# Optimization experiments

Hardware: AMD Instinct MI355X
Metric: run time of the kernel (lower is better)

The kernel has to match this reference:

```python
import jax, jax.numpy as jnp
import numpy as np

EPS = 1e-5

def ln(x, g, b):
    m = x.mean(-1, keepdims=True)
    v = ((x - m) ** 2).mean(-1, keepdims=True)
    return (x - m) / jnp.sqrt(v + EPS) * g + b

def mha(x, in_w, in_b, out_w, out_b, nh):
    # Faithful nn.MultiheadAttention with batch_first=False: x is (L, B, D),
    # attention runs over axis 0 (sequence), axis 1 is batch.
    L, Bb, D = x.shape
    hd = D // nh
    qkv = x @ in_w.T + in_b                      # (L, B, 3D)
    q, k, v = jnp.split(qkv, 3, axis=-1)
    q = q.reshape(L, Bb, nh, hd) * (hd ** -0.5)
    k = k.reshape(L, Bb, nh, hd)
    v = v.reshape(L, Bb, nh, hd)
    a = jax.nn.softmax(jnp.einsum('lbhe,sbhe->bhls', q, k), axis=-1)
    o = jnp.einsum('bhls,sbhe->lbhe', a, v).reshape(L, Bb, D)
    return o @ out_w.T + out_b

def psb_forward(features, prev_slots,
                lnq_g, lnq_b, lnkv_g, lnkv_b,
                wq, wk, wv, wo,
                lnt_g, lnt_b, t_in_w, t_in_b, t_out_w, t_out_b,
                lno_g, lno_b, o_in_w, o_in_b, o_out_w, o_out_b,
                lnp_g, lnp_b, w1, b1, w2, b2):
    B, T, L, D = features.shape
    N = prev_slots.shape[2]
    nh = 1                                        # inverse_nh
    hd = D // nh
    slots = ln(prev_slots, lnq_g, lnq_b).reshape(B * T, N, D)
    xkv = ln(features, lnkv_g, lnkv_b).reshape(B * T, L, D)
    # ---- inverse cross attention (softmax over query/slot dim, renorm over keys) ----
    q = (slots @ wq.T).reshape(B * T, N, nh, hd).transpose(0, 2, 1, 3) * (D ** -0.5)
    k = (xkv @ wk.T).reshape(B * T, L, nh, hd).transpose(0, 2, 1, 3)
    v = (xkv @ wv.T).reshape(B * T, L, nh, hd).transpose(0, 2, 1, 3)
    attn = jnp.einsum('bhnd,bhsd->bhns', q, k)    # (BT, nh, N, L)
    attn = jax.nn.softmax(attn, axis=-2)          # over slots (queries)
    attn = attn / attn.sum(-1, keepdims=True)     # renormalize over keys
    s = jnp.einsum('bhns,bhsd->bnhd', attn, v).reshape(B * T, N, D) @ wo.T
    # ---- time attention: input (B*T, N, D); seq axis 0 = B*T, batch = N ----
    s = ln(s, lnt_g, lnt_b)
    s = mha(s, t_in_w, t_in_b, t_out_w, t_out_b, 4)
    # rearrange '(b t) n d -> (b n) t d'
    s = s.reshape(B, T, N, D).transpose(0, 2, 1, 3).reshape(B * N, T, D)
    # ---- object attention: seq axis 0 = B*N, batch = T ----
    s = ln(s, lno_g, lno_b)
    s = mha(s, o_in_w, o_in_b, o_out_w, o_out_b, 4)
    # faithful to torch .view(B, T, N, D) on a contiguous (B*N, T, D) tensor:
    # raw row-major reinterpretation (same as torch)
    s = s.reshape(B, T, N, D)
    # ---- FFN projection + residual with prev_slots ----
    s = ln(s, lnp_g, lnp_b)
    s = jax.nn.relu(s @ w1.T + b1) @ w2.T + b2
    return s + prev_slots

def setup_inputs() -> dict:
    key = jax.random.key(0)
    ks = jax.random.split(key, 16)
    B, T, L, D, N, F = 8, 16, 1024, 192, 8, 512
    w = lambda k, shape: jax.random.normal(k, shape, jnp.float32) * 0.02
    return {
        'features': jax.random.normal(ks[0], (B, T, L, D), jnp.float32),
        'prev_slots': jax.random.normal(ks[1], (B, T, N, D), jnp.float32),
        'lnq_g': jnp.ones((D,), jnp.float32), 'lnq_b': jnp.zeros((D,), jnp.float32),
        'lnkv_g': jnp.ones((D,), jnp.float32), 'lnkv_b': jnp.zeros((D,), jnp.float32),
        'wq': w(ks[2], (D, D)), 'wk': w(ks[3], (D, D)),
        'wv': w(ks[4], (D, D)), 'wo': w(ks[5], (D, D)),
        'lnt_g': jnp.ones((D,), jnp.float32), 'lnt_b': jnp.zeros((D,), jnp.float32),
        't_in_w': w(ks[6], (3 * D, D)), 't_in_b': jnp.zeros((3 * D,), jnp.float32),
        't_out_w': w(ks[7], (D, D)), 't_out_b': jnp.zeros((D,), jnp.float32),
        'lno_g': jnp.ones((D,), jnp.float32), 'lno_b': jnp.zeros((D,), jnp.float32),
        'o_in_w': w(ks[8], (3 * D, D)), 'o_in_b': jnp.zeros((3 * D,), jnp.float32),
        'o_out_w': w(ks[9], (D, D)), 'o_out_b': jnp.zeros((D,), jnp.float32),
        'lnp_g': jnp.ones((D,), jnp.float32), 'lnp_b': jnp.zeros((D,), jnp.float32),
        'w1': w(ks[10], (F, D)), 'b1': jnp.zeros((F,), jnp.float32),
        'w2': w(ks[11], (D, F)), 'b2': jnp.zeros((D,), jnp.float32),
    }

def reference(features, prev_slots,
              lnq_g, lnq_b, lnkv_g, lnkv_b,
              wq, wk, wv, wo,
              lnt_g, lnt_b, t_in_w, t_in_b, t_out_w, t_out_b,
              lno_g, lno_b, o_in_w, o_in_b, o_out_w, o_out_b,
              lnp_g, lnp_b, w1, b1, w2, b2):
    return psb_forward(features, prev_slots,
                       lnq_g, lnq_b, lnkv_g, lnkv_b,
                       wq, wk, wv, wo,
                       lnt_g, lnt_b, t_in_w, t_in_b, t_out_w, t_out_b,
                       lno_g, lno_b, o_in_w, o_in_b, o_out_w, o_out_b,
                       lnp_g, lnp_b, w1, b1, w2, b2)
```

## Files before the change

### kernel.cpp

```cpp
#include <hip/hip_runtime.h>
#include <hip/hip_bf16.h>
#include <stdint.h>

typedef __hip_bfloat16 bf16;

__device__ __forceinline__ float b2f(bf16 x){ return __bfloat162float(x); }
__device__ __forceinline__ bf16  f2b(float x){ return __float2bfloat16(x); }
__device__ __forceinline__ float bfl(unsigned u){ return __uint_as_float(u << 16); }
__device__ __forceinline__ float bfh(unsigned u){ return __uint_as_float(u & 0xffff0000u); }
__device__ __forceinline__ int dflag(const void* rawg){
  return *(const uint32_t*)rawg == 0x3F803F80u;
}

struct Ptrs26 { const void* p[26]; };
__global__ __launch_bounds__(256) void k_prep(Ptrs26 ps, float* __restrict__ dst,
    float* __restrict__ M1, float* __restrict__ M2t, float* __restrict__ cM2)
{
  constexpr int kN[26] = {192,192,192,192, 36864,36864,36864,36864, 192,192,
                          110592,576, 36864,192, 192,192, 110592,576, 36864,192,
                          192,192, 98304,512, 98304,192};
  constexpr int kR[26] = {0,0,0,0, 0,0,0,0, 0,0,
                          576,0, 192,0, 0,0, 576,0, 192,0,
                          0,0, 512,0, 192,0};
  const int b = blockIdx.x, t = threadIdx.x;
  const int flag = dflag(ps.p[0]);
  if (b < 1941){
    int tz = 0, boff = 0, off = 0;
    for (int i = 0; i < 26; ++i){
      const int nb = (i >= 4 && i < 8) ? 0 : ((kN[i] + 255) >> 8);
      if (b < boff + nb){ tz = i; break; }
      boff += nb; off += kN[i];
    }
    const int cnt = kN[tz];
    const int tid = (b - boff)*256 + t;
    if (tid >= cnt) return;
    float v = flag ? b2f(((const bf16*)ps.p[tz])[tid]) : ((const float*)ps.p[tz])[tid];
    const int R = kR[tz];
    if (R == 0){
      dst[off + tid] = v;
    } else {
      const int K = cnt / R;
      int o = tid / K, e = tid - o*K;
      dst[off + e*R + o] = v;
    }
    return;
  }
  __shared__ float sred[3];
  const int bm = b - 1941;
  const int mat = bm >= 192;
  const int row = mat ? bm - 192 : bm;
  float acc = 0.f;
  if (t < 192){
    float aa = 0.f, ab = 0.f;
    if (!mat){
      if (flag){
        const bf16* wq = (const bf16*)ps.p[4]; const bf16* wk = (const bf16*)ps.p[5];
        for (int d = 0; d < 192; d += 2){
          aa += b2f(wq[d*192 + row])     * b2f(wk[d*192 + t]);
          ab += b2f(wq[(d+1)*192 + row]) * b2f(wk[(d+1)*192 + t]);
        }
      } else {
        const float* wq = (const float*)ps.p[4]; const float* wk = (const float*)ps.p[5];
        for (int d = 0; d < 192; d += 2){
          aa += wq[d*192 + row]*wk[d*192 + t];
          ab += wq[(d+1)*192 + row]*wk[(d+1)*192 + t];
        }
      }
      M1[row*192 + t] = (aa + ab) * 0.07216878364870323f;
    } else {
      if (flag){
        const bf16* wo = (const bf16*)ps.p[7]; const bf16* wv = (const bf16*)ps.p[6];
        for (int d = 0; d < 192; d += 2){
          aa += b2f(wo[row*192 + d])   * b2f(wv[d*192 + t]);
          ab += b2f(wo[row*192 + d+1]) * b2f(wv[(d+1)*192 + t]);
        }
      } else {
        const float* wo = (const float*)ps.p[7]; const float* wv = (const float*)ps.p[6];
        for (int d = 0; d < 192; d += 2){
          aa += wo[row*192 + d]  *wv[d*192 + t];
          ab += wo[row*192 + d+1]*wv[(d+1)*192 + t];
        }
      }
      acc = aa + ab;
      M2t[t*192 + row] = acc;
    }
  }
  if (mat){
    float bk = 0.f;
    if (t < 192) bk = flag ? b2f(((const bf16*)ps.p[3])[t]) : ((const float*)ps.p[3])[t];
    float c = (t < 192) ? acc*bk : 0.f;
    #pragma unroll
    for (int o = 32; o > 0; o >>= 1) c += __shfl_xor(c, o);
    if ((t & 63) == 0 && t < 192) sred[t >> 6] = c;
    __syncthreads();
    if (t == 0) cM2[row] = sred[0] + sred[1] + sred[2];
  }
}

__global__ __launch_bounds__(192) void k_qprime(
    const void* __restrict__ prev, const void* __restrict__ rawg,
    const float* __restrict__ g, const float* __restrict__ be,
    const float* __restrict__ gkv, const float* __restrict__ bkv,
    const float* __restrict__ M1, float* __restrict__ Qg, float* __restrict__ cS)
{
  __shared__ float sRaw[4][196];
  __shared__ float sS[4][196];
  __shared__ float sMS[4][2];
  __shared__ float sCred[3][4];
  const int t = threadIdx.x, bt = blockIdx.x;
  const int n0 = blockIdx.y*4;
  const int flag = dflag(rawg);
  #pragma unroll
  for (int r = 0; r < 4; ++r){
    size_t idx = ((size_t)bt*8 + n0 + r)*192 + t;
    sRaw[r][t] = flag ? b2f(((const bf16*)prev)[idx]) : ((const float*)prev)[idx];
  }
  __syncthreads();
  if (t < 4){
    float s = 0.f, q = 0.f;
    for (int e = 0; e < 192; ++e){ float x = sRaw[t][e]; s += x; q += x*x; }
    float m = s*(1.f/192.f);
    float rstd = rsqrtf(q*(1.f/192.f) - m*m + 1e-5f);
    sMS[t][0] = m; sMS[t][1] = rstd;
  }
  __syncthreads();
  const float gg = g[t], bb = be[t];
  #pragma unroll
  for (int r = 0; r < 4; ++r)
    sS[r][t] = (sRaw[r][t] - sMS[r][0])*sMS[r][1]*gg + bb;
  __syncthreads();
  float acc[4] = {};
  for (int f = 0; f < 192; ++f){
    float mv = M1[f*192 + t];
    #pragma unroll
    for (int n = 0; n < 4; ++n) acc[n] += sS[n][f]*mv;
  }
  const float gk = gkv[t], bk = bkv[t];
  float c[4];
  #pragma unroll
  for (int n = 0; n < 4; ++n) c[n] = acc[n]*bk;
  #pragma unroll
  for (int o = 32; o > 0; o >>= 1){
    #pragma unroll
    for (int n = 0; n < 4; ++n) c[n] += __shfl_xor(c[n], o);
  }
  if ((t & 63) == 0){
    #pragma unroll
    for (int n = 0; n < 4; ++n) sCred[t >> 6][n] = c[n];
  }
  #pragma unroll
  for (int n = 0; n < 4; ++n) Qg[(size_t)bt*1536 + (n0+n)*192 + t] = acc[n]*gk;
  __syncthreads();
  if (t < 4) cS[(size_t)bt*8 + n0 + t] = sCred[0][t] + sCred[1][t] + sCred[2][t];
}

__global__ __launch_bounds__(256) void k_front(
    const void* __restrict__ feat, const void* __restrict__ rawg,
    const float* __restrict__ Qg, const float* __restrict__ cSg,
    float* __restrict__ pP, float* __restrict__ pR)
{
  __shared__ float sQ[8][196];
  __shared__ float sX[16][200];
  __shared__ float sA[16][8];
  __shared__ float sRS[4][8];
  __shared__ float sCS[8];
  const int t = threadIdx.x, lane = t & 63, w = t >> 6;
  const int split = blockIdx.x, bt = blockIdx.y;
  const int flag = dflag(rawg);
  const int grp = lane >> 4, gl = lane & 15;
  const int lrow = w*4 + grp;
  const int le0  = gl*12;
  const int pc = t >> 3, pn = t & 7;
  const size_t rowbase = (size_t)bt*1024 + (size_t)split*64;

  float4 pf0, pf1, pf2;
  uint2  pb0, pb1, pb2;
  auto issue = [&](int tile){
    size_t ro = (rowbase + (size_t)(tile*16 + lrow))*192 + le0;
    if (flag){
      const uint2* p2 = (const uint2*)((const bf16*)feat + ro);
      pb0 = p2[0]; pb1 = p2[1]; pb2 = p2[2];
    } else {
      const float4* p4 = (const float4*)((const float*)feat + ro);
      pf0 = p4[0]; pf1 = p4[1]; pf2 = p4[2];
    }
  };
  issue(0);

  for (int i = t; i < 1536; i += 256){
    int n = i / 192, e = i - n*192;
    sQ[n][e] = Qg[(size_t)bt*1536 + i];
  }
  if (t < 8) sCS[t] = cSg[(size_t)bt*8 + t];
  float accP[8] = {0,0,0,0,0,0,0,0};
  float rs[8]   = {0,0,0,0,0,0,0,0};
  __syncthreads();

  for (int tile = 0; tile < 4; ++tile){
    float x[12];
    if (flag){
      x[0]=bfl(pb0.x); x[1]=bfh(pb0.x); x[2]=bfl(pb0.y); x[3]=bfh(pb0.y);
      x[4]=bfl(pb1.x); x[5]=bfh(pb1.x); x[6]=bfl(pb1.y); x[7]=bfh(pb1.y);
      x[8]=bfl(pb2.x); x[9]=bfh(pb2.x); x[10]=bfl(pb2.y); x[11]=bfh(pb2.y);
    } else {
      x[0]=pf0.x; x[1]=pf0.y; x[2]=pf0.z; x[3]=pf0.w;
      x[4]=pf1.x; x[5]=pf1.y; x[6]=pf1.z; x[7]=pf1.w;
      x[8]=pf2.x; x[9]=pf2.y; x[10]=pf2.z; x[11]=pf2.w;
    }
    if (tile < 3) issue(tile + 1);
    float s = 0.f, q = 0.f;
    #pragma unroll
    for (int j = 0; j < 12; ++j){ s += x[j]; q += x[j]*x[j]; }
    #pragma unroll
    for (int o = 1; o < 16; o <<= 1){ s += __shfl_xor(s, o); q += __shfl_xor(q, o); }
    float m = s*(1.f/192.f);
    float rstd = rsqrtf(q*(1.f/192.f) - m*m + 1e-5f);
    #pragma unroll
    for (int j = 0; j < 12; ++j) x[j] = (x[j]-m)*rstd;
    float p[8];
    #pragma unroll
    for (int n = 0; n < 8; ++n){
      const float* qr = &sQ[n][le0];
      float4 qa = *(const float4*)qr;
      float4 qb = *(const float4*)(qr+4);
      float4 qc = *(const float4*)(qr+8);
      p[n] = x[0]*qa.x + x[1]*qa.y + x[2]*qa.z + x[3]*qa.w
           + x[4]*qb.x + x[5]*qb.y + x[6]*qb.z + x[7]*qb.w
           + x[8]*qc.x + x[9]*qc.y + x[10]*qc.z + x[11]*qc.w;
    }
    #pragma unroll
    for (int o = 1; o < 16; o <<= 1){
      #pragma unroll
      for (int n = 0; n < 8; ++n) p[n] += __shfl_xor(p[n], o);
    }
    #pragma unroll
    for (int n = 0; n < 8; ++n) p[n] += sCS[n];
    float mx = p[0];
    #pragma unroll
    for (int n = 1; n < 8; ++n) mx = fmaxf(mx, p[n]);
    float sum = 0.f;
    #pragma unroll
    for (int n = 0; n < 8; ++n){ p[n] = __expf(p[n]-mx); sum += p[n]; }
    float inv = 1.f/sum;
    #pragma unroll
    for (int n = 0; n < 8; ++n) p[n] *= inv;
    __syncthreads();
    *(float4*)&sX[lrow][le0]   = make_float4(x[0],x[1],x[2],x[3]);
    *(float4*)&sX[lrow][le0+4] = make_float4(x[4],x[5],x[6],x[7]);
    *(float4*)&sX[lrow][le0+8] = make_float4(x[8],x[9],x[10],x[11]);
    if (gl == 0){
      *(float4*)&sA[lrow][0] = make_float4(p[0],p[1],p[2],p[3]);
      *(float4*)&sA[lrow][4] = make_float4(p[4],p[5],p[6],p[7]);
      #pragma unroll
      for (int n = 0; n < 8; ++n) rs[n] += p[n];
    }
    __syncthreads();
    if (t < 192){
      #pragma unroll 4
      for (int k2 = 0; k2 < 16; ++k2){
        float av = sA[k2][pn];
        const float* xp2 = &sX[k2][pc*8];
        float4 u0 = *(const float4*)(xp2);
        float4 u1 = *(const float4*)(xp2 + 4);
        accP[0] += av*u0.x; accP[1] += av*u0.y; accP[2] += av*u0.z; accP[3] += av*u0.w;
        accP[4] += av*u1.x; accP[5] += av*u1.y; accP[6] += av*u1.z; accP[7] += av*u1.w;
      }
    }
  }

  if (t < 192){
    float* pp = pP + (((size_t)bt*16 + split)*8 + pn)*192 + pc*8;
    *(float4*)pp       = make_float4(accP[0],accP[1],accP[2],accP[3]);
    *(float4*)(pp + 4) = make_float4(accP[4],accP[5],accP[6],accP[7]);
  }
  #pragma unroll
  for (int n = 0; n < 8; ++n){
    rs[n] += __shfl_xor(rs[n], 16);
    rs[n] += __shfl_xor(rs[n], 32);
  }
  if (lane == 0){
    *(float4*)&sRS[w][0] = make_float4(rs[0],rs[1],rs[2],rs[3]);
    *(float4*)&sRS[w][4] = make_float4(rs[4],rs[5],rs[6],rs[7]);
  }
  __syncthreads();
  if (t < 8) pR[((size_t)bt*16 + split)*8 + t] = sRS[0][t]+sRS[1][t]+sRS[2][t]+sRS[3][t];
}

__global__ __launch_bounds__(256) void k_finln(
    const float* __restrict__ pP, const float* __restrict__ pR, const float* __restrict__ M2t,
    const float* __restrict__ gkv, const float* __restrict__ cM2,
    const float* __restrict__ g, const float* __restrict__ be,
    const float* __restrict__ Wt, const float* __restrict__ bias, float* __restrict__ out)
{
  __shared__ float sP[2][196];
  __shared__ float sx[2][196];
  __shared__ float sInv[2];
  __shared__ float sredS[2][4], sredQ[2][4];
  const int t = threadIdx.x, lane = t & 63, w = t >> 6;
  const int r0 = blockIdx.x*2;
  const int kk = blockIdx.y;
  const int bt = r0 >> 3;
  for (int j = t; j < 384; j += 256){
    int rr = (j >= 192) ? 1 : 0;
    int e = j - rr*192;
    int n = (r0 + rr) & 7;
    const float* src = pP + (((size_t)bt*16)*8 + n)*192 + e;
    float v0=0.f,v1=0.f,v2=0.f,v3=0.f;
    #pragma unroll
    for (int s = 0; s < 16; s += 4){
      v0 += src[(size_t)s*1536];
      v1 += src[(size_t)(s+1)*1536];
      v2 += src[(size_t)(s+2)*1536];
      v3 += src[(size_t)(s+3)*1536];
    }
    sP[rr][e] = gkv[e] * ((v0+v1)+(v2+v3));
  }
  if (t < 2){
    int n = (r0 + t) & 7;
    float r = 0.f;
    #pragma unroll
    for (int s = 0; s < 16; ++s) r += pR[((size_t)bt*16 + s)*8 + n];
    sInv[t] = 1.f/r;
  }
  __syncthreads();
  float a0 = 0.f, a1 = 0.f;
  if (t < 192){
    float a0a=0.f,a0b=0.f,a0c=0.f,a0d=0.f, a1a=0.f,a1b=0.f,a1c=0.f,a1d=0.f;
    for (int e = 0; e < 192; e += 4){
      float w0 = M2t[e*192 + t],     w1 = M2t[(e+1)*192 + t];
      float w2 = M2t[(e+2)*192 + t], w3 = M2t[(e+3)*192 + t];
      a0a += sP[0][e]*w0;   a1a += sP[1][e]*w0;
      a0b += sP[0][e+1]*w1; a1b += sP[1][e+1]*w1;
      a0c += sP[0][e+2]*w2; a1c += sP[1][e+2]*w2;
      a0d += sP[0][e+3]*w3; a1d += sP[1][e+3]*w3;
    }
    const float cm = cM2[t];
    a0 = ((a0a+a0b)+(a0c+a0d))*sInv[0] + cm;
    a1 = ((a1a+a1b)+(a1c+a1d))*sInv[1] + cm;
    float s0 = a0, q0 = a0*a0, s1 = a1, q1 = a1*a1;
    #pragma unroll
    for (int o = 32; o > 0; o >>= 1){
      s0 += __shfl_xor(s0,o); q0 += __shfl_xor(q0,o);
      s1 += __shfl_xor(s1,o); q1 += __shfl_xor(q1,o);
    }
    if (lane == 0){ sredS[0][w]=s0; sredQ[0][w]=q0; sredS[1][w]=s1; sredQ[1][w]=q1; }
  }
  __syncthreads();
  if (t < 192){
    float s0 = sredS[0][0]+sredS[0][1]+sredS[0][2];
    float q0 = sredQ[0][0]+sredQ[0][1]+sredQ[0][2];
    float s1 = sredS[1][0]+sredS[1][1]+sredS[1][2];
    float q1 = sredQ[1][0]+sredQ[1][1]+sredQ[1][2];
    float m0 = s0*(1.f/192.f), m1 = s1*(1.f/192.f);
    float r0s = rsqrtf(q0*(1.f/192.f) - m0*m0 + 1e-5f);
    float r1s = rsqrtf(q1*(1.f/192.f) - m1*m1 + 1e-5f);
    float gg = g[t], bb = be[t];
    sx[0][t] = (a0 - m0)*r0s*gg + bb;
    sx[1][t] = (a1 - m1)*r1s*gg + bb;
  }
  __syncthreads();
  if (t < 192){
    const int o = t + kk*192;
    float c0a=0.f,c0b=0.f,c0c=0.f,c0d=0.f, c1a=0.f,c1b=0.f,c1c=0.f,c1d=0.f;
    for (int e = 0; e < 192; e += 4){
      float w0 = Wt[e*576 + o],     w1 = Wt[(e+1)*576 + o];
      float w2 = Wt[(e+2)*576 + o], w3 = Wt[(e+3)*576 + o];
      c0a += sx[0][e]*w0;   c1a += sx[1][e]*w0;
      c0b += sx[0][e+1]*w1; c1b += sx[1][e+1]*w1;
      c0c += sx[0][e+2]*w2; c1c += sx[1][e+2]*w2;
      c0d += sx[0][e+3]*w3; c1d += sx[1][e+3]*w3;
    }
    out[(size_t)r0*576 + o]     = ((c0a+c0b)+(c0c+c0d)) + bias[o];
    out[(size_t)(r0+1)*576 + o] = ((c1a+c1b)+(c1c+c1d)) + bias[o];
  }
}

__global__ __launch_bounds__(256) void k_attn8(
    const float* __restrict__ qkv, float* __restrict__ ao, int S, int B)
{
  __shared__ float sK[128][52];
  __shared__ float sV[128][52];
  __shared__ float sQ[8][52];
  __shared__ float sS[8][132];
  const int t = threadIdx.x;
  const int qt = blockIdx.x, h = blockIdx.y, b = blockIdx.z;
  const float sc = 0.1443375673f;
  for (int i = t; i < S*12; i += 256){
    int ks = i / 12, c = i - ks*12;
    const float* base = qkv + ((size_t)ks*B + b)*576 + h*48 + c*4;
    *(float4*)&sK[ks][c*4] = *(const float4*)(base + 192);
    *(float4*)&sV[ks][c*4] = *(const float4*)(base + 384);
  }
  if (t < 96){
    int qr = t / 12, c = t - qr*12;
    int lq = qt*8 + qr;
    float4 qv = *(const float4*)(qkv + ((size_t)lq*B + b)*576 + h*48 + c*4);
    qv.x *= sc; qv.y *= sc; qv.z *= sc; qv.w *= sc;
    *(float4*)&sQ[qr][c*4] = qv;
  }
  __syncthreads();
  const int qr = t >> 5, kk = t & 31;
  for (int ks = kk; ks < S; ks += 32){
    float acc = 0.f;
    #pragma unroll
    for (int j = 0; j < 12; ++j){
      float4 qv = *(const float4*)&sQ[qr][j*4];
      float4 kv = *(const float4*)&sK[ks][j*4];
      acc += qv.x*kv.x + qv.y*kv.y + qv.z*kv.z + qv.w*kv.w;
    }
    sS[qr][ks] = acc;
  }
  float mx = -1e30f;
  for (int ks = kk; ks < S; ks += 32) mx = fmaxf(mx, sS[qr][ks]);
  #pragma unroll
  for (int m = 1; m < 32; m <<= 1) mx = fmaxf(mx, __shfl_xor(mx, m));
  float sum = 0.f;
  for (int ks = kk; ks < S; ks += 32){
    float e = __expf(sS[qr][ks] - mx);
    sS[qr][ks] = e;
    sum += e;
  }
  #pragma unroll
  for (int m = 1; m < 32; m <<= 1) sum += __shfl_xor(sum, m);
  const float inv = 1.f / sum;
  __syncthreads();
  const int d0 = (kk & 15)*3;
  float a0 = 0.f, a1 = 0.f, a2 = 0.f, e0 = 0.f, e1 = 0.f, e2 = 0.f;
  for (int ks = (kk >> 4); ks < S; ks += 4){
    float p0 = sS[qr][ks], p1 = sS[qr][ks+2];
    a0 += p0*sV[ks][d0];   a1 += p0*sV[ks][d0+1];   a2 += p0*sV[ks][d0+2];
    e0 += p1*sV[ks+2][d0]; e1 += p1*sV[ks+2][d0+1]; e2 += p1*sV[ks+2][d0+2];
  }
  a0 += e0; a1 += e1; a2 += e2;
  a0 += __shfl_xor(a0, 16); a1 += __shfl_xor(a1, 16); a2 += __shfl_xor(a2, 16);
  if (kk < 16){
    const int lq = qt*8 + qr;
    float* op = ao + ((size_t)lq*B + b)*192 + h*48 + d0;
    op[0] = a0*inv; op[1] = a1*inv; op[2] = a2*inv;
  }
}

__global__ __launch_bounds__(256) void k_projln(
    const float* __restrict__ aoT, const float* __restrict__ W1t, const float* __restrict__ b1v,
    const float* __restrict__ g, const float* __restrict__ be,
    const float* __restrict__ Wt, const float* __restrict__ bias, float* __restrict__ out)
{
  __shared__ float sin[2][196];
  __shared__ float sx[2][196];
  __shared__ float sredS[2][4], sredQ[2][4];
  const int t = threadIdx.x, lane = t & 63, w = t >> 6;
  const int r0 = blockIdx.x*2;
  const int kk = blockIdx.y;
  if (t < 192){
    #pragma unroll
    for (int rr = 0; rr < 2; ++rr){
      int r = r0 + rr;
      int ls = r >> 4, tb = r & 15;
      int inrow = ((ls>>3)*16 + tb)*8 + (ls&7);
      sin[rr][t] = aoT[(size_t)inrow*192 + t];
    }
  }
  __syncthreads();
  float a0 = 0.f, a1 = 0.f;
  if (t < 192){
    float a0a=0.f,a0b=0.f,a0c=0.f,a0d=0.f, a1a=0.f,a1b=0.f,a1c=0.f,a1d=0.f;
    for (int e = 0; e < 192; e += 4){
      float w0 = W1t[e*192 + t],     w1 = W1t[(e+1)*192 + t];
      float w2 = W1t[(e+2)*192 + t], w3 = W1t[(e+3)*192 + t];
      a0a += sin[0][e]*w0;   a1a += sin[1][e]*w0;
      a0b += sin[0][e+1]*w1; a1b += sin[1][e+1]*w1;
      a0c += sin[0][e+2]*w2; a1c += sin[1][e+2]*w2;
      a0d += sin[0][e+3]*w3; a1d += sin[1][e+3]*w3;
    }
    a0 = ((a0a+a0b)+(a0c+a0d)) + b1v[t];
    a1 = ((a1a+a1b)+(a1c+a1d)) + b1v[t];
    float s0 = a0, q0 = a0*a0, s1 = a1, q1 = a1*a1;
    #pragma unroll
    for (int o = 32; o > 0; o >>= 1){
      s0 += __shfl_xor(s0,o); q0 += __shfl_xor(q0,o);
      s1 += __shfl_xor(s1,o); q1 += __shfl_xor(q1,o);
    }
    if (lane == 0){ sredS[0][w]=s0; sredQ[0][w]=q0; sredS[1][w]=s1; sredQ[1][w]=q1; }
  }
  __syncthreads();
  if (t < 192){
    float s0 = sredS[0][0]+sredS[0][1]+sredS[0][2];
    float q0 = sredQ[0][0]+sredQ[0][1]+sredQ[0][2];
    float s1 = sredS[1][0]+sredS[1][1]+sredS[1][2];
    float q1 = sredQ[1][0]+sredQ[1][1]+sredQ[1][2];
    float m0 = s0*(1.f/192.f), m1 = s1*(1.f/192.f);
    float r0s = rsqrtf(q0*(1.f/192.f) - m0*m0 + 1e-5f);
    float r1s = rsqrtf(q1*(1.f/192.f) - m1*m1 + 1e-5f);
    float gg = g[t], bb = be[t];
    sx[0][t] = (a0 - m0)*r0s*gg + bb;
    sx[1][t] = (a1 - m1)*r1s*gg + bb;
  }
  __syncthreads();
  if (t < 192){
    const int o = t + kk*192;
    float c0a=0.f,c0b=0.f,c0c=0.f,c0d=0.f, c1a=0.f,c1b=0.f,c1c=0.f,c1d=0.f;
    for (int e = 0; e < 192; e += 4){
      float w0 = Wt[e*576 + o],     w1 = Wt[(e+1)*576 + o];
      float w2 = Wt[(e+2)*576 + o], w3 = Wt[(e+3)*576 + o];
      c0a += sx[0][e]*w0;   c1a += sx[1][e]*w0;
      c0b += sx[0][e+1]*w1; c1b += sx[1][e+1]*w1;
      c0c += sx[0][e+2]*w2; c1c += sx[1][e+2]*w2;
      c0d += sx[0][e+3]*w3; c1d += sx[1][e+3]*w3;
    }
    out[(size_t)r0*576 + o]     = ((c0a+c0b)+(c0c+c0d)) + bias[o];
    out[(size_t)(r0+1)*576 + o] = ((c1a+c1b)+(c1c+c1d)) + bias[o];
  }
}

__global__ __launch_bounds__(256) void k_ffn2(
    const float* __restrict__ aoO, const float* __restrict__ Wpt, const float* __restrict__ bp,
    const float* __restrict__ g, const float* __restrict__ be,
    const float* __restrict__ w1t, const float* __restrict__ b1,
    const float* __restrict__ w2t, const float* __restrict__ b2,
    const void* __restrict__ prev, const void* __restrict__ rawg, void* __restrict__ out)
{
  __shared__ float sin[200];
  __shared__ float sx[200];
  __shared__ float sh[512];
  __shared__ float sredS[4], sredQ[4];
  const int t = threadIdx.x, lane = t & 63, w = t >> 6;
  const int r0 = blockIdx.x;
  const int flag = dflag(rawg);
  if (t < 192) sin[t] = aoO[(size_t)r0*192 + t];
  __syncthreads();
  float a0 = 0.f;
  if (t < 192){
    float aa=0.f, ab=0.f, ac=0.f, ad=0.f;
    for (int e = 0; e < 192; e += 4){
      aa += sin[e]  *Wpt[e*192 + t];
      ab += sin[e+1]*Wpt[(e+1)*192 + t];
      ac += sin[e+2]*Wpt[(e+2)*192 + t];
      ad += sin[e+3]*Wpt[(e+3)*192 + t];
    }
    a0 = ((aa+ab)+(ac+ad)) + bp[t];
    float s0 = a0, q0 = a0*a0;
    #pragma unroll
    for (int o = 32; o > 0; o >>= 1){ s0 += __shfl_xor(s0,o); q0 += __shfl_xor(q0,o); }
    if (lane == 0){ sredS[w]=s0; sredQ[w]=q0; }
  }
  __syncthreads();
  if (t < 192){
    float s0 = sredS[0]+sredS[1]+sredS[2];
    float q0 = sredQ[0]+sredQ[1]+sredQ[2];
    float m0 = s0*(1.f/192.f);
    float r0s = rsqrtf(q0*(1.f/192.f) - m0*m0 + 1e-5f);
    sx[t] = (a0 - m0)*r0s*g[t] + be[t];
  }
  __syncthreads();
  {
    float h0 = b1[t], h1 = b1[t+256], h0b = 0.f, h1b = 0.f;
    for (int e = 0; e < 192; e += 2){
      const float* wr0 = w1t + e*512;
      const float* wr1 = wr0 + 512;
      float x0 = sx[e], x1 = sx[e+1];
      h0  += x0*wr0[t]; h1  += x0*wr0[t+256];
      h0b += x1*wr1[t]; h1b += x1*wr1[t+256];
    }
    sh[t]     = fmaxf(h0 + h0b, 0.f);
    sh[t+256] = fmaxf(h1 + h1b, 0.f);
  }
  __syncthreads();
  if (t < 192){
    float ca=0.f, cb=0.f, cc=0.f, cd=0.f;
    for (int e = 0; e < 512; e += 4){
      ca += sh[e]  *w2t[e*192 + t];
      cb += sh[e+1]*w2t[(e+1)*192 + t];
      cc += sh[e+2]*w2t[(e+2)*192 + t];
      cd += sh[e+3]*w2t[(e+3)*192 + t];
    }
    float y = ((ca+cb)+(cc+cd)) + b2[t];
    size_t oi = (size_t)r0*192 + t;
    float res = flag ? b2f(((const bf16*)prev)[oi]) : ((const float*)prev)[oi];
    y += res;
    if (flag) ((bf16*)out)[oi] = f2b(y);
    else      ((float*)out)[oi] = y;
  }
}

extern "C" void kernel_launch(void* const* d_in, const int* in_sizes, int n_in,
                              void* d_out, int out_size, void* d_ws, size_t ws_size,
                              hipStream_t stream)
{
  const void* feat = d_in[0];
  const void* prev = d_in[1];
  const void* rawg = d_in[2];
  static const int kWN[26] = {192,192,192,192, 36864,36864,36864,36864, 192,192,
                              110592,576, 36864,192, 192,192, 110592,576, 36864,192,
                              192,192, 98304,512, 98304,192};
  Ptrs26 ps;
  for (int i = 0; i < 26; ++i) ps.p[i] = d_in[2 + i];

  float* wconv = (float*)d_ws;
  size_t woff[26]; size_t acc_ = 0;
  for (int i = 0; i < 26; ++i){ woff[i] = acc_; acc_ += kWN[i]; }
  float* M1   = wconv + 643136;
  float* M2t  = M1 + 36864;
  float* Qp   = M2t + 36864;
  float* pP   = Qp + 196608;
  float* pR   = pP + 3145728;
  float* qkvT = pR + 16384;
  float* aoT  = qkvT + 589824;
  float* qkvO = aoT + 196608;
  float* aoO  = qkvO + 589824;
  const size_t needed = (size_t)((char*)(aoO + 196608) - (char*)d_ws);
  if (ws_size < needed) return;
  float* cM2 = qkvO;
  float* cS  = aoO;

  const float* c_lnq_g  = wconv + woff[0];
  const float* c_lnq_b  = wconv + woff[1];
  const float* c_lnkv_g = wconv + woff[2];
  const float* c_lnkv_b = wconv + woff[3];
  const float* c_lnt_g  = wconv + woff[8];
  const float* c_lnt_b  = wconv + woff[9];
  const float* c_tin_w  = wconv + woff[10];
  const float* c_tin_b  = wconv + woff[11];
  const float* c_tout_w = wconv + woff[12];
  const float* c_tout_b = wconv + woff[13];
  const float* c_lno_g  = wconv + woff[14];
  const float* c_lno_b  = wconv + woff[15];
  const float* c_oin_w  = wconv + woff[16];
  const float* c_oin_b  = wconv + woff[17];
  const float* c_oout_w = wconv + woff[18];
  const float* c_oout_b = wconv + woff[19];
  const float* c_lnp_g  = wconv + woff[20];
  const float* c_lnp_b  = wconv + woff[21];
  const float* c_w1     = wconv + woff[22];
  const float* c_b1     = wconv + woff[23];
  const float* c_w2     = wconv + woff[24];
  const float* c_b2     = wconv + woff[25];

  k_prep<<<2325, 256, 0, stream>>>(ps, wconv, M1, M2t, cM2);
  k_qprime<<<dim3(128, 2), 192, 0, stream>>>(prev, rawg, c_lnq_g, c_lnq_b, c_lnkv_g,
                                             c_lnkv_b, M1, Qp, cS);
  k_front<<<dim3(16, 128), 256, 0, stream>>>(feat, rawg, Qp, cS, pP, pR);
  k_finln<<<dim3(512, 3), 256, 0, stream>>>(pP, pR, M2t, c_lnkv_g, cM2, c_lnt_g, c_lnt_b,
                                            c_tin_w, c_tin_b, qkvT);
  k_attn8<<<dim3(16,4,8), 256, 0, stream>>>(qkvT, aoT, 128, 8);
  k_projln<<<dim3(512, 3), 256, 0, stream>>>(aoT, c_tout_w, c_tout_b, c_lno_g, c_lno_b,
                                             c_oin_w, c_oin_b, qkvO);
  k_attn8<<<dim3(8,4,16), 256, 0, stream>>>(qkvO, aoO, 64, 16);
  k_ffn2<<<1024, 256, 0, stream>>>(aoO, c_oout_w, c_oout_b, c_lnp_g, c_lnp_b,
                                   c_w1, c_b1, c_w2, c_b2, prev, rawg, d_out);
}
```

Baseline: 342.9 us.

## Fuse tail kernels into one cooperative persistent kernel with grid syncs

Replaces the five tail launches (finln, time attention, projln, object attention, ffn2) with a single cooperative kernel of 1024 blocks that runs each stage in turn, separated by grid-wide syncs. The aim is to remove the launch gaps and tail drain between small kernels. The finln and projln stages now handle one row per block with 192 active threads, where before they used a 3-way column split across more blocks. This cuts parallelism inside those phases, and each grid.sync adds cost. If the cooperative launch fails, the code falls back to the old launches.

```diff
diff --git a/kernel.cpp b/kernel.cpp
--- a/kernel.cpp
+++ b/kernel.cpp
@@ -1,7 +1,9 @@
 #include <hip/hip_runtime.h>
+#include <hip/hip_cooperative_groups.h>
 #include <hip/hip_bf16.h>
 #include <stdint.h>
 
+namespace cg = cooperative_groups;
 typedef __hip_bfloat16 bf16;
 
 __device__ __forceinline__ float b2f(bf16 x){ return __bfloat162float(x); }
@@ -582,6 +584,261 @@
   }
 }
 
+struct TailArgs {
+  const float *pP, *pR, *M2t, *gkv, *cM2, *lnt_g, *lnt_b, *tin_w, *tin_b;
+  float *qkvT, *aoT;
+  const float *tout_w, *tout_b, *lno_g, *lno_b, *oin_w, *oin_b;
+  float *qkvO, *aoO;
+  const float *oout_w, *oout_b, *lnp_g, *lnp_b, *w1t, *b1, *w2t, *b2;
+  const void *prev, *rawg;
+  void *out;
+};
+
+__device__ void attn_phase(const float* __restrict__ qkv, float* __restrict__ ao,
+                           int S, int Batt, int qt, int h, int bb,
+                           float* smemf, int t)
+{
+  float (*sKV)[52] = (float(*)[52])smemf;
+  float (*sQ)[52]  = (float(*)[52])(smemf + 6656);
+  float (*sS)[132] = (float(*)[132])(smemf + 7072);
+  const float sc = 0.1443375673f;
+  for (int i = t; i < S*12; i += 256){
+    int ks = i / 12, c = i - ks*12;
+    const float* base = qkv + ((size_t)ks*Batt + bb)*576 + h*48 + c*4;
+    *(float4*)&sKV[ks][c*4] = *(const float4*)(base + 192);
+  }
+  if (t < 96){
+    int qr = t / 12, c = t - qr*12;
+    int lq = qt*8 + qr;
+    float4 qv = *(const float4*)(qkv + ((size_t)lq*Batt + bb)*576 + h*48 + c*4);
+    qv.x *= sc; qv.y *= sc; qv.z *= sc; qv.w *= sc;
+    *(float4*)&sQ[qr][c*4] = qv;
+  }
+  __syncthreads();
+  const int qr = t >> 5, kk = t & 31;
+  for (int ks = kk; ks < S; ks += 32){
+    float acc = 0.f;
+    #pragma unroll
+    for (int j = 0; j < 12; ++j){
+      float4 qv = *(const float4*)&sQ[qr][j*4];
+      float4 kv = *(const float4*)&sKV[ks][j*4];
+      acc += qv.x*kv.x + qv.y*kv.y + qv.z*kv.z + qv.w*kv.w;
+    }
+    sS[qr][ks] = acc;
+  }
+  __syncthreads();
+  for (int i = t; i < S*12; i += 256){
+    int ks = i / 12, c = i - ks*12;
+    const float* base = qkv + ((size_t)ks*Batt + bb)*576 + h*48 + c*4;
+    *(float4*)&sKV[ks][c*4] = *(const float4*)(base + 384);
+  }
+  float mx = -1e30f;
+  for (int ks = kk; ks < S; ks += 32) mx = fmaxf(mx, sS[qr][ks]);
+  #pragma unroll
+  for (int m = 1; m < 32; m <<= 1) mx = fmaxf(mx, __shfl_xor(mx, m));
+  float sum = 0.f;
+  for (int ks = kk; ks < S; ks += 32){
+    float e = __expf(sS[qr][ks] - mx);
+    sS[qr][ks] = e;
+    sum += e;
+  }
+  #pragma unroll
+  for (int m = 1; m < 32; m <<= 1) sum += __shfl_xor(sum, m);
+  const float inv = 1.f / sum;
+  __syncthreads();
+  const int d0 = (kk & 15)*3;
+  float a0=0.f,a1=0.f,a2=0.f,e0=0.f,e1=0.f,e2=0.f;
+  for (int ks = (kk >> 4); ks < S; ks += 4){
+    float p0 = sS[qr][ks], p1 = sS[qr][ks+2];
+    a0 += p0*sKV[ks][d0];   a1 += p0*sKV[ks][d0+1];   a2 += p0*sKV[ks][d0+2];
+    e0 += p1*sKV[ks+2][d0]; e1 += p1*sKV[ks+2][d0+1]; e2 += p1*sKV[ks+2][d0+2];
+  }
+  a0 += e0; a1 += e1; a2 += e2;
+  a0 += __shfl_xor(a0, 16); a1 += __shfl_xor(a1, 16); a2 += __shfl_xor(a2, 16);
+  if (kk < 16){
+    const int lq = qt*8 + qr;
+    float* op = ao + ((size_t)lq*Batt + bb)*192 + h*48 + d0;
+    op[0] = a0*inv; op[1] = a1*inv; op[2] = a2*inv;
+  }
+}
+
+__device__ void finln_row(const TailArgs& A, int r, float* smemf, int t, int lane, int w)
+{
+  float* sP = smemf; float* sx = smemf + 200; float* sred = smemf + 400; float* sInv = smemf + 408;
+  const int bt = r >> 3, n = r & 7;
+  if (t < 192){
+    const float* src = A.pP + (((size_t)bt*16)*8 + n)*192 + t;
+    float v0=0.f,v1=0.f,v2=0.f,v3=0.f;
+    #pragma unroll
+    for (int s = 0; s < 16; s += 4){
+      v0 += src[(size_t)s*1536];     v1 += src[(size_t)(s+1)*1536];
+      v2 += src[(size_t)(s+2)*1536]; v3 += src[(size_t)(s+3)*1536];
+    }
+    sP[t] = A.gkv[t] * ((v0+v1)+(v2+v3));
+  }
+  if (t == 0){
+    float rr = 0.f;
+    #pragma unroll
+    for (int s = 0; s < 16; ++s) rr += A.pR[((size_t)bt*16 + s)*8 + n];
+    sInv[0] = 1.f/rr;
+  }
+  __syncthreads();
+  float a = 0.f;
+  if (t < 192){
+    float a0=0.f,a1=0.f,a2=0.f,a3=0.f;
+    for (int e = 0; e < 192; e += 4){
+      a0 += sP[e]  *A.M2t[e*192 + t];     a1 += sP[e+1]*A.M2t[(e+1)*192 + t];
+      a2 += sP[e+2]*A.M2t[(e+2)*192 + t]; a3 += sP[e+3]*A.M2t[(e+3)*192 + t];
+    }
+    a = ((a0+a1)+(a2+a3))*sInv[0] + A.cM2[t];
+    float s = a, q = a*a;
+    #pragma unroll
+    for (int o = 32; o > 0; o >>= 1){ s += __shfl_xor(s,o); q += __shfl_xor(q,o); }
+    if (lane == 0){ sred[w] = s; sred[4+w] = q; }
+  }
+  __syncthreads();
+  if (t < 192){
+    float s0 = sred[0]+sred[1]+sred[2], q0 = sred[4]+sred[5]+sred[6];
+    float m = s0*(1.f/192.f);
+    float rstd = rsqrtf(q0*(1.f/192.f) - m*m + 1e-5f);
+    sx[t] = (a - m)*rstd*A.lnt_g[t] + A.lnt_b[t];
+  }
+  __syncthreads();
+  if (t < 192){
+    #pragma unroll
+    for (int k = 0; k < 3; ++k){
+      const int o = t + k*192;
+      float c0=0.f,c1=0.f,c2=0.f,c3=0.f;
+      for (int e = 0; e < 192; e += 4){
+        c0 += sx[e]  *A.tin_w[e*576 + o];     c1 += sx[e+1]*A.tin_w[(e+1)*576 + o];
+        c2 += sx[e+2]*A.tin_w[(e+2)*576 + o]; c3 += sx[e+3]*A.tin_w[(e+3)*576 + o];
+      }
+      A.qkvT[(size_t)r*576 + o] = ((c0+c1)+(c2+c3)) + A.tin_b[o];
+    }
+  }
+}
+
+__device__ void projln_row(const TailArgs& A, int r, float* smemf, int t, int lane, int w)
+{
+  float* sin = smemf; float* sx = smemf + 200; float* sred = smemf + 400;
+  if (t < 192){
+    int ls = r >> 4, tb = r & 15;
+    int inrow = ((ls>>3)*16 + tb)*8 + (ls&7);
+    sin[t] = A.aoT[(size_t)inrow*192 + t];
+  }
+  __syncthreads();
+  float a = 0.f;
+  if (t < 192){
+    float a0=0.f,a1=0.f,a2=0.f,a3=0.f;
+    for (int e = 0; e < 192; e += 4){
+      a0 += sin[e]  *A.tout_w[e*192 + t];     a1 += sin[e+1]*A.tout_w[(e+1)*192 + t];
+      a2 += sin[e+2]*A.tout_w[(e+2)*192 + t]; a3 += sin[e+3]*A.tout_w[(e+3)*192 + t];
+    }
+    a = ((a0+a1)+(a2+a3)) + A.tout_b[t];
+    float s = a, q = a*a;
+    #pragma unroll
+    for (int o = 32; o > 0; o >>= 1){ s += __shfl_xor(s,o); q += __shfl_xor(q,o); }
+    if (lane == 0){ sred[w] = s; sred[4+w] = q; }
+  }
+  __syncthreads();
+  if (t < 192){
+    float s0 = sred[0]+sred[1]+sred[2], q0 = sred[4]+sred[5]+sred[6];
+    float m = s0*(1.f/192.f);
+    float rstd = rsqrtf(q0*(1.f/192.f) - m*m + 1e-5f);
+    sx[t] = (a - m)*rstd*A.lno_g[t] + A.lno_b[t];
+  }
+  __syncthreads();
+  if (t < 192){
+    #pragma unroll
+    for (int k = 0; k < 3; ++k){
+      const int o = t + k*192;
+      float c0=0.f,c1=0.f,c2=0.f,c3=0.f;
+      for (int e = 0; e < 192; e += 4){
+        c0 += sx[e]  *A.oin_w[e*576 + o];     c1 += sx[e+1]*A.oin_w[(e+1)*576 + o];
+        c2 += sx[e+2]*A.oin_w[(e+2)*576 + o]; c3 += sx[e+3]*A.oin_w[(e+3)*576 + o];
+      }
+      A.qkvO[(size_t)r*576 + o] = ((c0+c1)+(c2+c3)) + A.oin_b[o];
+    }
+  }
+}
+
+__device__ void ffn2_row(const TailArgs& A, int r, float* smemf, int t, int lane, int w, int flag)
+{
+  float* sin = smemf; float* sx = smemf + 200; float* sh = smemf + 400; float* sred = smemf + 912;
+  if (t < 192) sin[t] = A.aoO[(size_t)r*192 + t];
+  __syncthreads();
+  float a0 = 0.f;
+  if (t < 192){
+    float aa=0.f, ab=0.f, ac=0.f, ad=0.f;
+    for (int e = 0; e < 192; e += 4){
+      aa += sin[e]  *A.oout_w[e*192 + t];
+      ab += sin[e+1]*A.oout_w[(e+1)*192 + t];
+      ac += sin[e+2]*A.oout_w[(e+2)*192 + t];
+      ad += sin[e+3]*A.oout_w[(e+3)*192 + t];
+    }
+    a0 = ((aa+ab)+(ac+ad)) + A.oout_b[t];
+    float s0 = a0, q0 = a0*a0;
+    #pragma unroll
+    for (int o = 32; o > 0; o >>= 1){ s0 += __shfl_xor(s0,o); q0 += __shfl_xor(q0,o); }
+    if (lane == 0){ sred[w] = s0; sred[4+w] = q0; }
+  }
+  __syncthreads();
+  if (t < 192){
+    float s0 = sred[0]+sred[1]+sred[2];
+    float q0 = sred[4]+sred[5]+sred[6];
+    float m0 = s0*(1.f/192.f);
+    float r0s = rsqrtf(q0*(1.f/192.f) - m0*m0 + 1e-5f);
+    sx[t] = (a0 - m0)*r0s*A.lnp_g[t] + A.lnp_b[t];
+  }
+  __syncthreads();
+  {
+    float h0 = A.b1[t], h1 = A.b1[t+256], h0b = 0.f, h1b = 0.f;
+    for (int e = 0; e < 192; e += 2){
+      const float* wr0 = A.w1t + e*512;
+      const float* wr1 = wr0 + 512;
+      float x0 = sx[e], x1 = sx[e+1];
+      h0  += x0*wr0[t]; h1  += x0*wr0[t+256];
+      h0b += x1*wr1[t]; h1b += x1*wr1[t+256];
+    }
+    sh[t]     = fmaxf(h0 + h0b, 0.f);
+    sh[t+256] = fmaxf(h1 + h1b, 0.f);
+  }
+  __syncthreads();
+  if (t < 192){
+    float ca=0.f, cb=0.f, cc=0.f, cd=0.f;
+    for (int e = 0; e < 512; e += 4){
+      ca += sh[e]  *A.w2t[e*192 + t];
+      cb += sh[e+1]*A.w2t[(e+1)*192 + t];
+      cc += sh[e+2]*A.w2t[(e+2)*192 + t];
+      cd += sh[e+3]*A.w2t[(e+3)*192 + t];
+    }
+    float y = ((ca+cb)+(cc+cd)) + A.b2[t];
+    size_t oi = (size_t)r*192 + t;
+    float res = flag ? b2f(((const bf16*)A.prev)[oi]) : ((const float*)A.prev)[oi];
+    y += res;
+    if (flag) ((bf16*)A.out)[oi] = f2b(y);
+    else      ((float*)A.out)[oi] = y;
+  }
+}
+
+__global__ __launch_bounds__(256, 4) void k_tail(TailArgs A)
+{
+  __shared__ __align__(16) float smemf[8128];
+  cg::grid_group grid = cg::this_grid();
+  const int b = blockIdx.x, t = threadIdx.x, lane = t & 63, w = t >> 6;
+  const int flag = dflag(A.rawg);
+
+  finln_row(A, b, smemf, t, lane, w);
+  grid.sync();
+  if (b < 512) attn_phase(A.qkvT, A.aoT, 128, 8, b & 15, (b>>4)&3, b>>6, smemf, t);
+  grid.sync();
+  projln_row(A, b, smemf, t, lane, w);
+  grid.sync();
+  if (b < 512) attn_phase(A.qkvO, A.aoO, 64, 16, b & 7, (b>>3)&3, b>>5, smemf, t);
+  grid.sync();
+  ffn2_row(A, b, smemf, t, lane, w, flag);
+}
+
 extern "C" void kernel_launch(void* const* d_in, const int* in_sizes, int n_in,
                               void* d_out, int out_size, void* d_ws, size_t ws_size,
                               hipStream_t stream)
@@ -639,12 +896,29 @@
   k_qprime<<<dim3(128, 2), 192, 0, stream>>>(prev, rawg, c_lnq_g, c_lnq_b, c_lnkv_g,
                                              c_lnkv_b, M1, Qp, cS);
   k_front<<<dim3(16, 128), 256, 0, stream>>>(feat, rawg, Qp, cS, pP, pR);
-  k_finln<<<dim3(512, 3), 256, 0, stream>>>(pP, pR, M2t, c_lnkv_g, cM2, c_lnt_g, c_lnt_b,
-                                            c_tin_w, c_tin_b, qkvT);
-  k_attn8<<<dim3(16,4,8), 256, 0, stream>>>(qkvT, aoT, 128, 8);
-  k_projln<<<dim3(512, 3), 256, 0, stream>>>(aoT, c_tout_w, c_tout_b, c_lno_g, c_lno_b,
-                                             c_oin_w, c_oin_b, qkvO);
-  k_attn8<<<dim3(8,4,16), 256, 0, stream>>>(qkvO, aoO, 64, 16);
-  k_ffn2<<<1024, 256, 0, stream>>>(aoO, c_oout_w, c_oout_b, c_lnp_g, c_lnp_b,
-                                   c_w1, c_b1, c_w2, c_b2, prev, rawg, d_out);
-}
+
+  TailArgs ta;
+  ta.pP = pP; ta.pR = pR; ta.M2t = M2t; ta.gkv = c_lnkv_g; ta.cM2 = cM2;
+  ta.lnt_g = c_lnt_g; ta.lnt_b = c_lnt_b; ta.tin_w = c_tin_w; ta.tin_b = c_tin_b;
+  ta.qkvT = qkvT; ta.aoT = aoT;
+  ta.tout_w = c_tout_w; ta.tout_b = c_tout_b; ta.lno_g = c_lno_g; ta.lno_b = c_lno_b;
+  ta.oin_w = c_oin_w; ta.oin_b = c_oin_b;
+  ta.qkvO = qkvO; ta.aoO = aoO;
+  ta.oout_w = c_oout_w; ta.oout_b = c_oout_b; ta.lnp_g = c_lnp_g; ta.lnp_b = c_lnp_b;
+  ta.w1t = c_w1; ta.b1 = c_b1; ta.w2t = c_w2; ta.b2 = c_b2;
+  ta.prev = prev; ta.rawg = rawg; ta.out = d_out;
+  void* kargs[] = { &ta };
+  hipError_t cerr = hipLaunchCooperativeKernel(reinterpret_cast<void*>(k_tail),
+                                               dim3(1024), dim3(256), kargs, 0, stream);
+  if (cerr != hipSuccess){
+    (void)hipGetLastError();
+    k_finln<<<dim3(512, 3), 256, 0, stream>>>(pP, pR, M2t, c_lnkv_g, cM2, c_lnt_g, c_lnt_b,
+                                              c_tin_w, c_tin_b, qkvT);
+    k_attn8<<<dim3(16,4,8), 256, 0, stream>>>(qkvT, aoT, 128, 8);
+    k_projln<<<dim3(512, 3), 256, 0, stream>>>(aoT, c_tout_w, c_tout_b, c_lno_g, c_lno_b,
+                                               c_oin_w, c_oin_b, qkvO);
+    k_attn8<<<dim3(8,4,16), 256, 0, stream>>>(qkvO, aoO, 64, 16);
+    k_ffn2<<<1024, 256, 0, stream>>>(aoO, c_oout_w, c_oout_b, c_lnp_g, c_lnp_b,
+                                     c_w1, c_b1, c_w2, c_b2, prev, rawg, d_out);
+  }
+}
```

Result: slower. 850.2 us (+147.9%).
